# Optimization experiments

Hardware: AMD Instinct MI355X
Metric: run time of the kernel (lower is better)

## Reference

```python
import jax, jax.numpy as jnp
import numpy as np

DIM = 192
HEADS = 8
EPS = 1e-12

def conv2d(x, w, groups=1, padding='SAME'):
    return jax.lax.conv_general_dilated(
        x, w, window_strides=(1, 1), padding=padding,
        dimension_numbers=('NCHW', 'OIHW', 'NCHW'),
        feature_group_count=groups)

def setup_inputs() -> dict:
    key = jax.random.key(0)
    ks = jax.random.split(key, 6)
    b, c, h, w = 8, DIM, 128, 128
    x = jax.random.normal(ks[0], (b, c, h, w), dtype=jnp.float32)
    # depthwise 3x3 conv on x (groups=dim): OIHW with I=1
    w_dw = jax.random.normal(ks[1], (DIM, 1, 3, 3), dtype=jnp.float32) * 0.1
    # 1x1 qkv projection
    w_qkv = jax.random.normal(ks[2], (DIM * 3, DIM, 1, 1), dtype=jnp.float32) * (1.0 / np.sqrt(DIM))
    # depthwise 3x3 on qkv (groups=3*dim)
    w_qkvdw = jax.random.normal(ks[3], (DIM * 3, 1, 3, 3), dtype=jnp.float32) * 0.1
    # 1x1 output projection
    w_proj = jax.random.normal(ks[4], (DIM, DIM, 1, 1), dtype=jnp.float32) * (1.0 / np.sqrt(DIM))
    temperature = jnp.ones((HEADS, 1, 1), dtype=jnp.float32)
    rescale = jnp.ones((HEADS, 1), dtype=jnp.float32)
    return {"x": x, "w_dw": w_dw, "w_qkv": w_qkv, "w_qkvdw": w_qkvdw,
            "w_proj": w_proj, "temperature": temperature, "rescale": rescale}

def l2norm_lastdim(t):
    # matches F.normalize(t, dim=-1, eps=1e-12)
    n = jnp.sqrt(jnp.sum(t * t, axis=-1, keepdims=True))
    return t / jnp.maximum(n, EPS)

def reference(x, w_dw, w_qkv, w_qkvdw, w_proj, temperature, rescale):
    b, c, h, w = x.shape
    heads = HEADS
    c_head = c // heads
    # variance (unbiased, like torch.var default) of depthwise-conv features over H,W
    xd = conv2d(x, w_dw, groups=c)                      # [b,c,h,w]
    var = jnp.var(xd, axis=(-2, -1), ddof=1)            # [b,c]
    var = var.reshape(b, heads, c_head)                 # [b,head,c_head]
    # qkv: 1x1 conv then depthwise 3x3
    qkv = conv2d(conv2d(x, w_qkv), w_qkvdw, groups=3 * c)  # [b,3c,h,w]
    q, k, v = jnp.split(qkv, 3, axis=1)
    def to_heads(t):
        return t.reshape(b, heads, c_head, h * w)       # b head c (h w)
    q, k, v = to_heads(q), to_heads(k), to_heads(v)
    q = l2norm_lastdim(q)
    k = l2norm_lastdim(k)
    # channel attention: [b,head,c_head,c_head]
    attn = jnp.einsum('bhcn,bhdn->bhcd', q, k) * temperature
    # diagonal bias from variance, scaled per-head
    diag = rescale * var                                # [b,head,c_head]
    attn = attn + jnp.einsum('bhc,cd->bhcd', diag, jnp.eye(c_head, dtype=attn.dtype))
    attn = jax.nn.softmax(attn, axis=-1)
    out = jnp.einsum('bhcd,bhdn->bhcn', attn, v)        # [b,head,c_head,hw]
    out = out.reshape(b, c, h, w)
    return conv2d(out, w_proj)
```

## Files before the change

kernel.cpp:

```cpp
#include <hip/hip_runtime.h>
#include <hip/hip_bf16.h>

typedef unsigned short ushort_t;
typedef __bf16 bf16x8 __attribute__((ext_vector_type(8)));
typedef float f32x4 __attribute__((ext_vector_type(4)));
typedef unsigned short us8 __attribute__((ext_vector_type(8)));
typedef unsigned short us4 __attribute__((ext_vector_type(4)));

#define HW 16384
#define CDIM 192
#define QKVC 576

static __device__ __forceinline__ float b2f(unsigned short u) {
    union { unsigned int i; float f; } cv; cv.i = ((unsigned int)u) << 16; return cv.f;
}
static __device__ __forceinline__ unsigned short f2b(float f) {
    union { __bf16 h; unsigned short u; } cv; cv.h = (__bf16)f; return cv.u;
}

__global__ __launch_bounds__(256) void k_cvt(const float* __restrict__ src,
                                             ushort_t* __restrict__ dst, int n8) {
    int i = blockIdx.x * 256 + threadIdx.x;
    if (i >= n8) return;
    f32x4 a = *(const f32x4*)&src[i * 8];
    f32x4 b = *(const f32x4*)&src[i * 8 + 4];
    us8 o;
#pragma unroll
    for (int e = 0; e < 4; ++e) { o[e] = f2b(a[e]); o[4 + e] = f2b(b[e]); }
    *(us8*)&dst[i * 8] = o;
}

__global__ __launch_bounds__(256) void k_dwvar(const float* __restrict__ x,
                                               const float* __restrict__ wdw,
                                               float* __restrict__ vs1,
                                               float* __restrict__ vs2,
                                               ushort_t* __restrict__ xb) {
    __shared__ __align__(16) float pl[66 * 132];
    __shared__ float red[8];
    int blk = blockIdx.x;
    int bc = blk >> 1, half = blk & 1, rb = half * 64;
    int c = bc % CDIM;
    const float* xp = x + (size_t)bc * HW;
    ushort_t* xbp = xb + (size_t)bc * HW;
    int t = threadIdx.x;
#pragma unroll
    for (int i = 0; i < 8; ++i) {
        int gi = t + i * 256;
        int row = gi >> 5, q4 = (gi & 31) * 4;
        f32x4 v4 = *(const f32x4*)&xp[(size_t)(rb + row) * 128 + q4];
        *(f32x4*)&pl[(row + 1) * 132 + q4] = v4;
        us4 b4;
#pragma unroll
        for (int j = 0; j < 4; ++j) b4[j] = f2b(v4[j]);
        *(us4*)&xbp[(size_t)(rb + row) * 128 + q4] = b4;
    }
    if (t < 32) {
        f32x4 v = {0.f, 0.f, 0.f, 0.f};
        if (rb > 0) v = *(const f32x4*)&xp[(size_t)(rb - 1) * 128 + t * 4];
        *(f32x4*)&pl[t * 4] = v;
    } else if (t < 64) {
        int g = t - 32;
        f32x4 v = {0.f, 0.f, 0.f, 0.f};
        if (rb + 64 < 128) v = *(const f32x4*)&xp[(size_t)(rb + 64) * 128 + g * 4];
        *(f32x4*)&pl[65 * 132 + g * 4] = v;
    }
    float w[9];
#pragma unroll
    for (int j = 0; j < 9; ++j) w[j] = wdw[c * 9 + j];
    __syncthreads();

    int lane = t & 63, wv = t >> 6;
    int y = lane, xs = wv * 32;
    int yb0 = y * 132, yb1 = yb0 + 132, yb2 = yb1 + 132;
    float l0 = 0.f, l1 = 0.f, l2 = 0.f;
    if (xs != 0) {
        f32x4 h0 = *(const f32x4*)&pl[yb0 + xs - 4];
        f32x4 h1 = *(const f32x4*)&pl[yb1 + xs - 4];
        f32x4 h2 = *(const f32x4*)&pl[yb2 + xs - 4];
        l0 = h0[3]; l1 = h1[3]; l2 = h2[3];
    }
    f32x4 a0 = *(const f32x4*)&pl[yb0 + xs], b0 = *(const f32x4*)&pl[yb0 + xs + 4];
    f32x4 a1 = *(const f32x4*)&pl[yb1 + xs], b1 = *(const f32x4*)&pl[yb1 + xs + 4];
    f32x4 a2 = *(const f32x4*)&pl[yb2 + xs], b2 = *(const f32x4*)&pl[yb2 + xs + 4];
    float s1 = 0.f, s2 = 0.f;
#pragma unroll
    for (int g = 0; g < 4; ++g) {
        int x0 = xs + g * 8;
        f32x4 na0, nb0, na1, nb1, na2, nb2;
        float e9_0, e9_1, e9_2;
        if (g < 3) {
            na0 = *(const f32x4*)&pl[yb0 + x0 + 8]; nb0 = *(const f32x4*)&pl[yb0 + x0 + 12];
            na1 = *(const f32x4*)&pl[yb1 + x0 + 8]; nb1 = *(const f32x4*)&pl[yb1 + x0 + 12];
            na2 = *(const f32x4*)&pl[yb2 + x0 + 8]; nb2 = *(const f32x4*)&pl[yb2 + x0 + 12];
            e9_0 = na0[0]; e9_1 = na1[0]; e9_2 = na2[0];
        } else {
            e9_0 = e9_1 = e9_2 = 0.f;
            if (xs + 32 < 128) {
                f32x4 q0 = *(const f32x4*)&pl[yb0 + xs + 32];
                f32x4 q1 = *(const f32x4*)&pl[yb1 + xs + 32];
                f32x4 q2 = *(const f32x4*)&pl[yb2 + xs + 32];
                e9_0 = q0[0]; e9_1 = q1[0]; e9_2 = q2[0];
            }
        }
        float e0[10], e1[10], e2[10];
        e0[0] = l0; e1[0] = l1; e2[0] = l2;
#pragma unroll
        for (int j = 0; j < 4; ++j) {
            e0[1 + j] = a0[j]; e0[5 + j] = b0[j];
            e1[1 + j] = a1[j]; e1[5 + j] = b1[j];
            e2[1 + j] = a2[j]; e2[5 + j] = b2[j];
        }
        e0[9] = e9_0; e1[9] = e9_1; e2[9] = e9_2;
#pragma unroll
        for (int j = 0; j < 8; ++j) {
            float o = e0[j] * w[0] + e0[j + 1] * w[1] + e0[j + 2] * w[2]
                    + e1[j] * w[3] + e1[j + 1] * w[4] + e1[j + 2] * w[5]
                    + e2[j] * w[6] + e2[j + 1] * w[7] + e2[j + 2] * w[8];
            s1 += o; s2 += o * o;
        }
        l0 = e0[8]; l1 = e1[8]; l2 = e2[8];
        if (g < 3) { a0 = na0; b0 = nb0; a1 = na1; b1 = nb1; a2 = na2; b2 = nb2; }
    }
#pragma unroll
    for (int off = 32; off; off >>= 1) { s1 += __shfl_xor(s1, off); s2 += __shfl_xor(s2, off); }
    if (lane == 0) { red[wv * 2] = s1; red[wv * 2 + 1] = s2; }
    __syncthreads();
    if (t == 0) {
        atomicAdd(&vs1[bc], red[0] + red[2] + red[4] + red[6]);
        atomicAdd(&vs2[bc], red[1] + red[3] + red[5] + red[7]);
    }
}

__global__ __launch_bounds__(256) void k_dwqkv(const ushort_t* __restrict__ qkvraw,
                                               const float* __restrict__ wqd,
                                               ushort_t* __restrict__ qkvd,
                                               float* __restrict__ ssq) {
    __shared__ __align__(16) ushort_t pl[66 * 136];
    __shared__ float red[4];
    int blk = blockIdx.x;
    int bo = blk >> 1, half = blk & 1, rb = half * 64;
    int o = bo % QKVC, b = bo / QKVC;
    const ushort_t* xp = qkvraw + (size_t)bo * HW;
    ushort_t* op = qkvd + (size_t)bo * HW;
    int t = threadIdx.x;
#pragma unroll
    for (int i = 0; i < 4; ++i) {
        int gi = t + i * 256;
        int row = gi >> 4, gr = (gi & 15) * 8;
        *(us8*)&pl[(row + 1) * 136 + gr] = *(const us8*)&xp[(size_t)(rb + row) * 128 + gr];
    }
    if (t < 16) {
        us8 v = {};
        if (rb > 0) v = *(const us8*)&xp[(size_t)(rb - 1) * 128 + t * 8];
        *(us8*)&pl[t * 8] = v;
    } else if (t < 32) {
        int g = t - 16;
        us8 v = {};
        if (rb + 64 < 128) v = *(const us8*)&xp[(size_t)(rb + 64) * 128 + g * 8];
        *(us8*)&pl[65 * 136 + g * 8] = v;
    }
    float w[9];
#pragma unroll
    for (int j = 0; j < 9; ++j) w[j] = wqd[o * 9 + j];
    __syncthreads();

    int lane = t & 63, wv = t >> 6;
    int y = lane, xs = wv * 32;
    int yb0 = y * 136, yb1 = yb0 + 136, yb2 = yb1 + 136;
    float l0 = 0.f, l1 = 0.f, l2 = 0.f;
    if (xs != 0) {
        us8 h0 = *(const us8*)&pl[yb0 + xs - 8];
        us8 h1 = *(const us8*)&pl[yb1 + xs - 8];
        us8 h2 = *(const us8*)&pl[yb2 + xs - 8];
        l0 = b2f(h0[7]); l1 = b2f(h1[7]); l2 = b2f(h2[7]);
    }
    us8 c0 = *(const us8*)&pl[yb0 + xs];
    us8 c1 = *(const us8*)&pl[yb1 + xs];
    us8 c2 = *(const us8*)&pl[yb2 + xs];
    float s2 = 0.f;
#pragma unroll
    for (int g = 0; g < 4; ++g) {
        int x0 = xs + g * 8;
        us8 n0, n1, n2;
        float e9_0, e9_1, e9_2;
        if (g < 3) {
            n0 = *(const us8*)&pl[yb0 + x0 + 8];
            n1 = *(const us8*)&pl[yb1 + x0 + 8];
            n2 = *(const us8*)&pl[yb2 + x0 + 8];
            e9_0 = b2f(n0[0]); e9_1 = b2f(n1[0]); e9_2 = b2f(n2[0]);
        } else {
            e9_0 = e9_1 = e9_2 = 0.f;
            if (xs + 32 < 128) {
                us8 q0 = *(const us8*)&pl[yb0 + xs + 32];
                us8 q1 = *(const us8*)&pl[yb1 + xs + 32];
                us8 q2 = *(const us8*)&pl[yb2 + xs + 32];
                e9_0 = b2f(q0[0]); e9_1 = b2f(q1[0]); e9_2 = b2f(q2[0]);
            }
        }
        float e0[10], e1[10], e2[10];
        e0[0] = l0; e1[0] = l1; e2[0] = l2;
#pragma unroll
        for (int j = 0; j < 8; ++j) { e0[j + 1] = b2f(c0[j]); e1[j + 1] = b2f(c1[j]); e2[j + 1] = b2f(c2[j]); }
        e0[9] = e9_0; e1[9] = e9_1; e2[9] = e9_2;
        us8 ob;
#pragma unroll
        for (int j = 0; j < 8; ++j) {
            float ov = e0[j] * w[0] + e0[j + 1] * w[1] + e0[j + 2] * w[2]
                     + e1[j] * w[3] + e1[j + 1] * w[4] + e1[j + 2] * w[5]
                     + e2[j] * w[6] + e2[j + 1] * w[7] + e2[j + 2] * w[8];
            ob[j] = f2b(ov);
            s2 += ov * ov;
        }
        *(us8*)&op[(size_t)(rb + y) * 128 + x0] = ob;
        l0 = e0[8]; l1 = e1[8]; l2 = e2[8];
        if (g < 3) { c0 = n0; c1 = n1; c2 = n2; }
    }
#pragma unroll
    for (int off = 32; off; off >>= 1) s2 += __shfl_xor(s2, off);
    if (lane == 0) red[wv] = s2;
    __syncthreads();
    if (t == 0 && o < 2 * CDIM)
        atomicAdd(&ssq[b * 384 + o], red[0] + red[1] + red[2] + red[3]);
}

template<int CF>
__global__ __launch_bounds__(256) void k_gemm(const ushort_t* __restrict__ Av, long sAb,
                                              const ushort_t* __restrict__ Bv, long sBb,
                                              void* __restrict__ Cv, long sCb, int K) {
    __shared__ __align__(16) char smem[49152];
    ushort_t* As = (ushort_t*)smem;
    ushort_t* Bs = (ushort_t*)(smem + 24576);
    int t = threadIdx.x;
    int wv = t >> 6, lane = t & 63, quad = lane >> 4, l15 = lane & 15;
    size_t aoff = (size_t)blockIdx.z * sAb + (size_t)blockIdx.y * 192 * K;
    size_t boff = (size_t)blockIdx.z * sBb + (size_t)blockIdx.x * 128;
    size_t coff = (size_t)blockIdx.z * sCb + (size_t)blockIdx.y * 192 * HW + (size_t)blockIdx.x * 128;
    f32x4 acc[24] = {};
    int bkr = t >> 3, bn0 = (t & 7) * 16, tlow = t & 7;
    int gk0 = bkr >> 3, klo = bkr & 7;
    const ushort_t* Bp = Bv + boff;
    us8 pb0 = *(const us8*)&Bp[(size_t)bkr * HW + bn0];
    us8 pb1 = *(const us8*)&Bp[(size_t)bkr * HW + bn0 + 8];
    us8 pb2 = *(const us8*)&Bp[(size_t)(bkr + 32) * HW + bn0];
    us8 pb3 = *(const us8*)&Bp[(size_t)(bkr + 32) * HW + bn0 + 8];
    int nIter = K >> 6;
    for (int it = 0; it < nIter; ++it) {
        int kk = it << 6;
#pragma unroll
        for (int i = 0; i < 6; ++i) {
            int s = t + i * 256;
            int row = s >> 3, kc = (s & 7) * 8;
            int kcs = kc ^ ((row & 7) * 8);
            *(uint4*)&As[row * 64 + kcs] = *(const uint4*)&Av[aoff + (size_t)row * K + kk + kc];
        }
#pragma unroll
        for (int e = 0; e < 8; ++e) {
            int col0 = ((gk0 ^ tlow ^ e) << 3) + klo;
            Bs[(bn0 + e) * 64 + col0] = pb0[e];
            Bs[(bn0 + 8 + e) * 64 + col0] = pb1[e];
            int col1 = (((gk0 + 4) ^ tlow ^ e) << 3) + klo;
            Bs[(bn0 + e) * 64 + col1] = pb2[e];
            Bs[(bn0 + 8 + e) * 64 + col1] = pb3[e];
        }
        __syncthreads();
        if (it + 1 < nIter) {
            const ushort_t* Bn = &Bp[(size_t)(kk + 64) * HW];
            pb0 = *(const us8*)&Bn[(size_t)bkr * HW + bn0];
            pb1 = *(const us8*)&Bn[(size_t)bkr * HW + bn0 + 8];
            pb2 = *(const us8*)&Bn[(size_t)(bkr + 32) * HW + bn0];
            pb3 = *(const us8*)&Bn[(size_t)(bkr + 32) * HW + bn0 + 8];
        }
#pragma unroll
        for (int s = 0; s < 2; ++s) {
            int r0 = wv * 16 + l15, r1 = 64 + r0, r2 = 128 + r0;
            int ko = s * 32 + quad * 8;
            bf16x8 af0 = *(const bf16x8*)&As[r0 * 64 + (ko ^ ((r0 & 7) * 8))];
            bf16x8 af1 = *(const bf16x8*)&As[r1 * 64 + (ko ^ ((r1 & 7) * 8))];
            bf16x8 af2 = *(const bf16x8*)&As[r2 * 64 + (ko ^ ((r2 & 7) * 8))];
#pragma unroll
            for (int tc = 0; tc < 8; ++tc) {
                int n = tc * 16 + l15;
                int g = (s * 4 + quad) ^ ((tc ^ l15) & 7);
                bf16x8 bfr = *(const bf16x8*)&Bs[n * 64 + (g << 3)];
                acc[tc]      = __builtin_amdgcn_mfma_f32_16x16x32_bf16(af0, bfr, acc[tc],      0, 0, 0);
                acc[8 + tc]  = __builtin_amdgcn_mfma_f32_16x16x32_bf16(af1, bfr, acc[8 + tc],  0, 0, 0);
                acc[16 + tc] = __builtin_amdgcn_mfma_f32_16x16x32_bf16(af2, bfr, acc[16 + tc], 0, 0, 0);
            }
        }
        __syncthreads();
    }
    if (CF == 0) {
        ushort_t* Ct = (ushort_t*)smem;
#pragma unroll
        for (int rt = 0; rt < 3; ++rt)
#pragma unroll
            for (int tc = 0; tc < 8; ++tc)
#pragma unroll
                for (int r = 0; r < 4; ++r)
                    Ct[(rt * 64 + wv * 16 + quad * 4 + r) * 128 + tc * 16 + l15] = f2b(acc[rt * 8 + tc][r]);
        __syncthreads();
        ushort_t* Co = (ushort_t*)Cv;
#pragma unroll
        for (int i = 0; i < 12; ++i) {
            int s = t + i * 256;
            int row = s >> 4, c8 = (s & 15) * 8;
            *(us8*)&Co[coff + (size_t)row * HW + c8] = *(us8*)&Ct[row * 128 + c8];
        }
    } else {
        float* Cf = (float*)smem;
        float* Co = (float*)Cv;
#pragma unroll
        for (int rt = 0; rt < 3; ++rt) {
            if (rt) __syncthreads();
#pragma unroll
            for (int tc = 0; tc < 8; ++tc)
#pragma unroll
                for (int r = 0; r < 4; ++r)
                    Cf[(wv * 16 + quad * 4 + r) * 128 + tc * 16 + l15] = acc[rt * 8 + tc][r];
            __syncthreads();
#pragma unroll
            for (int i = 0; i < 8; ++i) {
                int s = t + i * 256;
                int row = s >> 5, c4 = (s & 31) * 4;
                *(f32x4*)&Co[coff + (size_t)(rt * 64 + row) * HW + c4] = *(f32x4*)&Cf[row * 128 + c4];
            }
        }
    }
}

__global__ __launch_bounds__(256) void k_gram(const ushort_t* __restrict__ qkvd,
                                              float* __restrict__ G) {
    __shared__ __align__(16) ushort_t qs[24 * 264];
    __shared__ __align__(16) ushort_t ks[24 * 264];
    int bh = blockIdx.y;
    int b = bh >> 3, h = bh & 7;
    int t = threadIdx.x, wv = t >> 6, lane = t & 63, quad = lane >> 4, l15 = lane & 15;
    const ushort_t* qb = qkvd + (size_t)b * 9437184 + (size_t)(h * 24) * HW;
    const ushort_t* kp = qb + (size_t)CDIM * HW;
    f32x4 a00 = {}, a01 = {}, a10 = {}, a11 = {};
    bf16x8 z = {};
    bool hi = (l15 < 8);
    int kbase0 = blockIdx.x * 2048;
    for (int sub = 0; sub < 8; ++sub) {
        int kbase = kbase0 + sub * 256;
#pragma unroll
        for (int j = 0; j < 3; ++j) {
            int gi = t + j * 256;
            int row = gi >> 5, c8 = (gi & 31) * 8;
            *(us8*)&qs[row * 264 + c8] = *(const us8*)&qb[(size_t)row * HW + kbase + c8];
            *(us8*)&ks[row * 264 + c8] = *(const us8*)&kp[(size_t)row * HW + kbase + c8];
        }
        __syncthreads();
#pragma unroll
        for (int s = 0; s < 2; ++s) {
            int ko = (wv * 2 + s) * 32 + quad * 8;
            bf16x8 qa0 = *(const bf16x8*)&qs[l15 * 264 + ko];
            bf16x8 qa1 = hi ? *(const bf16x8*)&qs[(16 + l15) * 264 + ko] : z;
            bf16x8 kb0 = *(const bf16x8*)&ks[l15 * 264 + ko];
            bf16x8 kb1 = hi ? *(const bf16x8*)&ks[(16 + l15) * 264 + ko] : z;
            a00 = __builtin_amdgcn_mfma_f32_16x16x32_bf16(qa0, kb0, a00, 0, 0, 0);
            a01 = __builtin_amdgcn_mfma_f32_16x16x32_bf16(qa0, kb1, a01, 0, 0, 0);
            a10 = __builtin_amdgcn_mfma_f32_16x16x32_bf16(qa1, kb0, a10, 0, 0, 0);
            a11 = __builtin_amdgcn_mfma_f32_16x16x32_bf16(qa1, kb1, a11, 0, 0, 0);
        }
        __syncthreads();
    }
    float* Gp = G + (size_t)bh * 576;
#pragma unroll
    for (int r = 0; r < 4; ++r) {
        int r0 = quad * 4 + r, r1 = 16 + quad * 4 + r;
        int c0 = l15, c1 = 16 + l15;
        atomicAdd(&Gp[r0 * 24 + c0], a00[r]);
        if (c1 < 24) atomicAdd(&Gp[r0 * 24 + c1], a01[r]);
        if (r1 < 24) atomicAdd(&Gp[r1 * 24 + c0], a10[r]);
        if (r1 < 24 && c1 < 24) atomicAdd(&Gp[r1 * 24 + c1], a11[r]);
    }
}

__global__ __launch_bounds__(256) void k_smweff(const float* __restrict__ G,
                                                const float* __restrict__ ssq,
                                                const float* __restrict__ vs1,
                                                const float* __restrict__ vs2,
                                                const float* __restrict__ wproj,
                                                const float* __restrict__ temp,
                                                const float* __restrict__ resc,
                                                ushort_t* __restrict__ Weff) {
    int b = blockIdx.x, t = threadIdx.x;
    __shared__ float P[8 * 24 * 24];
    __shared__ float snq[192], snk[192];
    if (t < 192) {
        snq[t] = fmaxf(sqrtf(ssq[b * 384 + t]), 1e-12f);
        snk[t] = fmaxf(sqrtf(ssq[b * 384 + 192 + t]), 1e-12f);
    }
    __syncthreads();
    if (t < 192) {
        int h = t / 24, c = t % 24;
        float tmpv = temp[h];
        float S1 = vs1[b * 192 + t], S2 = vs2[b * 192 + t];
        float varv = (S2 - S1 * S1 * (1.0f / 16384.f)) * (1.0f / 16383.f);
        float dvar = resc[h] * varv;
        const float* Gp = G + (size_t)(b * 8 + h) * 576 + c * 24;
        float inq = tmpv / snq[t];
        float lg[24]; float mx = -1e30f;
#pragma unroll
        for (int d = 0; d < 24; ++d) {
            float v = Gp[d] * inq / snk[h * 24 + d];
            if (d == c) v += dvar;
            lg[d] = v; mx = fmaxf(mx, v);
        }
        float sum = 0.f;
#pragma unroll
        for (int d = 0; d < 24; ++d) { float e = __expf(lg[d] - mx); lg[d] = e; sum += e; }
        float inv = 1.f / sum;
#pragma unroll
        for (int d = 0; d < 24; ++d) P[(h * 24 + c) * 24 + d] = lg[d] * inv;
    }
    __syncthreads();
#pragma unroll
    for (int i = 0; i < 6; ++i) {
        int idx = t + (blockIdx.y * 6 + i) * 256;
        int co = idx / 192, hd = idx % 192;
        int h2 = hd / 24, d = hd % 24;
        float a = 0.f;
#pragma unroll
        for (int c2 = 0; c2 < 24; ++c2)
            a += wproj[co * 192 + h2 * 24 + c2] * P[(h2 * 24 + c2) * 24 + d];
        Weff[(size_t)b * 36864 + idx] = f2b(a);
    }
}

extern "C" void kernel_launch(void* const* d_in, const int* in_sizes, int n_in,
                              void* d_out, int out_size, void* d_ws, size_t ws_size,
                              hipStream_t stream) {
    const float* x      = (const float*)d_in[0];
    const float* wdw    = (const float*)d_in[1];
    const float* wqkv   = (const float*)d_in[2];
    const float* wqkvdw = (const float*)d_in[3];
    const float* wproj  = (const float*)d_in[4];
    const float* temp   = (const float*)d_in[5];
    const float* resc   = (const float*)d_in[6];
    float* out = (float*)d_out;

    char* ws = (char*)d_ws;
    ushort_t* qkvraw = (ushort_t*)ws;
    ushort_t* qkvd   = (ushort_t*)(ws + 150994944);
    char* small = ws + 301989888;
    float* vs1  = (float*)small;
    float* vs2  = (float*)(small + 6144);
    float* ssq  = (float*)(small + 12288);
    float* G    = (float*)(small + 24576);
    ushort_t* Weff = (ushort_t*)(small + 172032);

    ushort_t* xb  = qkvd;
    ushort_t* wqb = qkvd + 60000000;

    (void)hipMemsetAsync(small, 0, 172032, stream);
    k_cvt<<<dim3(54), dim3(256), 0, stream>>>(wqkv, wqb, 13824);
    k_dwvar<<<dim3(3072), dim3(256), 0, stream>>>(x, wdw, vs1, vs2, xb);
    k_gemm<0><<<dim3(128, 3, 8), dim3(256), 0, stream>>>(wqb, 0L, xb, 3145728L, qkvraw, 9437184L, 192);
    k_dwqkv<<<dim3(9216), dim3(256), 0, stream>>>(qkvraw, wqkvdw, qkvd, ssq);
    k_gram<<<dim3(8, 64), dim3(256), 0, stream>>>(qkvd, G);
    k_smweff<<<dim3(8, 24), dim3(256), 0, stream>>>(G, ssq, vs1, vs2, wproj, temp, resc, Weff);
    k_gemm<1><<<dim3(128, 1, 8), dim3(256), 0, stream>>>(Weff, 36864L, qkvd + (size_t)384 * HW, 9437184L, out, 3145728L, 192);
}
```

Before: 362.7 us.

## Fuse q/k depthwise conv into Gram kernel, restrict dwconv pass to v

The depthwise 3x3 conv for q and k channels now runs inside the Gram-matrix kernel, which loads row bands with halo from the raw qkv buffer, convolves them in shared memory, accumulates sum-of-squares, and feeds MFMA directly. The separate depthwise kernel now only processes the v third of the channels. This removes the write and re-read of the convolved q/k tensors (about two thirds of the dwconv output traffic) in exchange for halo reloads, shared-memory atomics and more syncs per band in the fused kernel.

Result: slower. 391.5 us (+7.9%).

```diff
diff --git a/kernel.cpp b/kernel.cpp
--- a/kernel.cpp
+++ b/kernel.cpp
@@ -131,15 +131,15 @@
     }
 }
 
-__global__ __launch_bounds__(256) void k_dwqkv(const ushort_t* __restrict__ qkvraw,
-                                               const float* __restrict__ wqd,
-                                               ushort_t* __restrict__ qkvd,
-                                               float* __restrict__ ssq) {
+__global__ __launch_bounds__(256) void k_dwv(const ushort_t* __restrict__ qkvraw,
+                                             const float* __restrict__ wqd,
+                                             ushort_t* __restrict__ qkvd) {
     __shared__ __align__(16) ushort_t pl[66 * 136];
-    __shared__ float red[4];
     int blk = blockIdx.x;
-    int bo = blk >> 1, half = blk & 1, rb = half * 64;
-    int o = bo % QKVC, b = bo / QKVC;
+    int pv = blk >> 1, half = blk & 1, rb = half * 64;
+    int b = pv / 192, ol = pv - b * 192;
+    int o = 384 + ol;
+    int bo = b * 576 + o;
     const ushort_t* xp = qkvraw + (size_t)bo * HW;
     ushort_t* op = qkvd + (size_t)bo * HW;
     int t = threadIdx.x;
@@ -177,7 +177,6 @@
     us8 c0 = *(const us8*)&pl[yb0 + xs];
     us8 c1 = *(const us8*)&pl[yb1 + xs];
     us8 c2 = *(const us8*)&pl[yb2 + xs];
-    float s2 = 0.f;
 #pragma unroll
     for (int g = 0; g < 4; ++g) {
         int x0 = xs + g * 8;
@@ -209,18 +208,127 @@
                      + e1[j] * w[3] + e1[j + 1] * w[4] + e1[j + 2] * w[5]
                      + e2[j] * w[6] + e2[j + 1] * w[7] + e2[j + 2] * w[8];
             ob[j] = f2b(ov);
-            s2 += ov * ov;
         }
         *(us8*)&op[(size_t)(rb + y) * 128 + x0] = ob;
         l0 = e0[8]; l1 = e1[8]; l2 = e2[8];
         if (g < 3) { c0 = n0; c1 = n1; c2 = n2; }
     }
-#pragma unroll
-    for (int off = 32; off; off >>= 1) s2 += __shfl_xor(s2, off);
-    if (lane == 0) red[wv] = s2;
+}
+
+__global__ __launch_bounds__(256) void k_qkgram(const ushort_t* __restrict__ qkvraw,
+                                                const float* __restrict__ wqd,
+                                                float* __restrict__ G,
+                                                float* __restrict__ ssq) {
+    __shared__ __align__(16) ushort_t in[48 * 4 * 128];
+    __shared__ float wl[48 * 9];
+    __shared__ float ssql[48];
+    ushort_t* qt = in;
+    ushort_t* kt = in + 24 * 264;
+    int band = blockIdx.x;
+    int bh = blockIdx.y;
+    int b = bh >> 3, h = bh & 7;
+    int t = threadIdx.x, wv = t >> 6, lane = t & 63, quad = lane >> 4, l15 = lane & 15;
+    bool hi = (l15 < 8);
+    bf16x8 z = {};
+    f32x4 a00 = {}, a01 = {}, a10 = {}, a11 = {};
+    if (t < 48) ssql[t] = 0.f;
+    for (int j = t; j < 432; j += 256) {
+        int p = j / 9, kk = j - p * 9;
+        int o = (p < 24) ? (h * 24 + p) : (192 + h * 24 + (p - 24));
+        wl[j] = wqd[o * 9 + kk];
+    }
+    const ushort_t* base = qkvraw + (size_t)b * 9437184;
+
+    for (int it2 = 0; it2 < 4; ++it2) {
+        __syncthreads();
+        int r0 = band * 8 + it2 * 2;
+#pragma unroll
+        for (int i = 0; i < 12; ++i) {
+            int gg = t + i * 256;
+            int p = gg >> 6, rem = gg & 63, ri = rem >> 4, gx = rem & 15;
+            int o = (p < 24) ? (h * 24 + p) : (192 + h * 24 + (p - 24));
+            int gr = r0 - 1 + ri;
+            us8 v = {};
+            if (gr >= 0 && gr < 128)
+                v = *(const us8*)&base[(size_t)o * HW + (size_t)gr * 128 + gx * 8];
+            *(us8*)&in[(p * 4 + ri) * 128 + gx * 8] = v;
+        }
+        __syncthreads();
+        us8 pa0, pa1, pa2, pa3, pa4, pa5;
+#pragma unroll
+        for (int i = 0; i < 6; ++i) {
+            int g = t + i * 256;
+            int s = g >> 4, p = s >> 1, orow = s & 1, x0 = (g & 15) * 8;
+            int rb0 = (p * 4 + orow) * 128;
+            us8 v0 = *(const us8*)&in[rb0 + x0];
+            us8 v1 = *(const us8*)&in[rb0 + 128 + x0];
+            us8 v2 = *(const us8*)&in[rb0 + 256 + x0];
+            float e0[10], e1[10], e2[10];
+            e0[0] = (x0 > 0) ? b2f(in[rb0 + x0 - 1]) : 0.f;
+            e1[0] = (x0 > 0) ? b2f(in[rb0 + 128 + x0 - 1]) : 0.f;
+            e2[0] = (x0 > 0) ? b2f(in[rb0 + 256 + x0 - 1]) : 0.f;
+#pragma unroll
+            for (int j = 0; j < 8; ++j) { e0[j + 1] = b2f(v0[j]); e1[j + 1] = b2f(v1[j]); e2[j + 1] = b2f(v2[j]); }
+            e0[9] = (x0 < 120) ? b2f(in[rb0 + x0 + 8]) : 0.f;
+            e1[9] = (x0 < 120) ? b2f(in[rb0 + 128 + x0 + 8]) : 0.f;
+            e2[9] = (x0 < 120) ? b2f(in[rb0 + 256 + x0 + 8]) : 0.f;
+            float w0 = wl[p * 9 + 0], w1 = wl[p * 9 + 1], w2 = wl[p * 9 + 2];
+            float w3 = wl[p * 9 + 3], w4 = wl[p * 9 + 4], w5 = wl[p * 9 + 5];
+            float w6 = wl[p * 9 + 6], w7 = wl[p * 9 + 7], w8 = wl[p * 9 + 8];
+            us8 ob;
+            float s2g = 0.f;
+#pragma unroll
+            for (int j = 0; j < 8; ++j) {
+                float ov = e0[j] * w0 + e0[j + 1] * w1 + e0[j + 2] * w2
+                         + e1[j] * w3 + e1[j + 1] * w4 + e1[j + 2] * w5
+                         + e2[j] * w6 + e2[j + 1] * w7 + e2[j + 2] * w8;
+                ob[j] = f2b(ov);
+                s2g += ov * ov;
+            }
+            atomicAdd(&ssql[p], s2g);
+            if (i == 0) pa0 = ob; else if (i == 1) pa1 = ob; else if (i == 2) pa2 = ob;
+            else if (i == 3) pa3 = ob; else if (i == 4) pa4 = ob; else pa5 = ob;
+        }
+        __syncthreads();
+#pragma unroll
+        for (int i = 0; i < 6; ++i) {
+            int g = t + i * 256;
+            int s = g >> 4, p = s >> 1, orow = s & 1, x0 = (g & 15) * 8;
+            us8 ob = (i == 0) ? pa0 : (i == 1) ? pa1 : (i == 2) ? pa2
+                   : (i == 3) ? pa3 : (i == 4) ? pa4 : pa5;
+            ushort_t* dst = (p < 24) ? qt : kt;
+            int cc = (p < 24) ? p : (p - 24);
+            *(us8*)&dst[cc * 264 + orow * 128 + x0] = ob;
+        }
+        __syncthreads();
+#pragma unroll
+        for (int s = 0; s < 2; ++s) {
+            int ko = (wv * 2 + s) * 32 + quad * 8;
+            bf16x8 qa0 = *(const bf16x8*)&qt[l15 * 264 + ko];
+            bf16x8 qa1 = hi ? *(const bf16x8*)&qt[(16 + l15) * 264 + ko] : z;
+            bf16x8 kb0 = *(const bf16x8*)&kt[l15 * 264 + ko];
+            bf16x8 kb1 = hi ? *(const bf16x8*)&kt[(16 + l15) * 264 + ko] : z;
+            a00 = __builtin_amdgcn_mfma_f32_16x16x32_bf16(qa0, kb0, a00, 0, 0, 0);
+            a01 = __builtin_amdgcn_mfma_f32_16x16x32_bf16(qa0, kb1, a01, 0, 0, 0);
+            a10 = __builtin_amdgcn_mfma_f32_16x16x32_bf16(qa1, kb0, a10, 0, 0, 0);
+            a11 = __builtin_amdgcn_mfma_f32_16x16x32_bf16(qa1, kb1, a11, 0, 0, 0);
+        }
+    }
+    float* Gp = G + (size_t)bh * 576;
+#pragma unroll
+    for (int r = 0; r < 4; ++r) {
+        int rr0 = quad * 4 + r, rr1 = 16 + quad * 4 + r;
+        int cc0 = l15, cc1 = 16 + l15;
+        atomicAdd(&Gp[rr0 * 24 + cc0], a00[r]);
+        if (cc1 < 24) atomicAdd(&Gp[rr0 * 24 + cc1], a01[r]);
+        if (rr1 < 24) atomicAdd(&Gp[rr1 * 24 + cc0], a10[r]);
+        if (rr1 < 24 && cc1 < 24) atomicAdd(&Gp[rr1 * 24 + cc1], a11[r]);
+    }
     __syncthreads();
-    if (t == 0 && o < 2 * CDIM)
-        atomicAdd(&ssq[b * 384 + o], red[0] + red[1] + red[2] + red[3]);
+    if (t < 48) {
+        int idx = (t < 24) ? (b * 384 + h * 24 + t) : (b * 384 + 192 + h * 24 + (t - 24));
+        atomicAdd(&ssq[idx], ssql[t]);
+    }
 }
 
 template<int CF>
@@ -328,55 +436,6 @@
     }
 }
 
-__global__ __launch_bounds__(256) void k_gram(const ushort_t* __restrict__ qkvd,
-                                              float* __restrict__ G) {
-    __shared__ __align__(16) ushort_t qs[24 * 264];
-    __shared__ __align__(16) ushort_t ks[24 * 264];
-    int bh = blockIdx.y;
-    int b = bh >> 3, h = bh & 7;
-    int t = threadIdx.x, wv = t >> 6, lane = t & 63, quad = lane >> 4, l15 = lane & 15;
-    const ushort_t* qb = qkvd + (size_t)b * 9437184 + (size_t)(h * 24) * HW;
-    const ushort_t* kp = qb + (size_t)CDIM * HW;
-    f32x4 a00 = {}, a01 = {}, a10 = {}, a11 = {};
-    bf16x8 z = {};
-    bool hi = (l15 < 8);
-    int kbase0 = blockIdx.x * 2048;
-    for (int sub = 0; sub < 8; ++sub) {
-        int kbase = kbase0 + sub * 256;
-#pragma unroll
-        for (int j = 0; j < 3; ++j) {
-            int gi = t + j * 256;
-            int row = gi >> 5, c8 = (gi & 31) * 8;
-            *(us8*)&qs[row * 264 + c8] = *(const us8*)&qb[(size_t)row * HW + kbase + c8];
-            *(us8*)&ks[row * 264 + c8] = *(const us8*)&kp[(size_t)row * HW + kbase + c8];
-        }
-        __syncthreads();
-#pragma unroll
-        for (int s = 0; s < 2; ++s) {
-            int ko = (wv * 2 + s) * 32 + quad * 8;
-            bf16x8 qa0 = *(const bf16x8*)&qs[l15 * 264 + ko];
-            bf16x8 qa1 = hi ? *(const bf16x8*)&qs[(16 + l15) * 264 + ko] : z;
-            bf16x8 kb0 = *(const bf16x8*)&ks[l15 * 264 + ko];
-            bf16x8 kb1 = hi ? *(const bf16x8*)&ks[(16 + l15) * 264 + ko] : z;
-            a00 = __builtin_amdgcn_mfma_f32_16x16x32_bf16(qa0, kb0, a00, 0, 0, 0);
-            a01 = __builtin_amdgcn_mfma_f32_16x16x32_bf16(qa0, kb1, a01, 0, 0, 0);
-            a10 = __builtin_amdgcn_mfma_f32_16x16x32_bf16(qa1, kb0, a10, 0, 0, 0);
-            a11 = __builtin_amdgcn_mfma_f32_16x16x32_bf16(qa1, kb1, a11, 0, 0, 0);
-        }
-        __syncthreads();
-    }
-    float* Gp = G + (size_t)bh * 576;
-#pragma unroll
-    for (int r = 0; r < 4; ++r) {
-        int r0 = quad * 4 + r, r1 = 16 + quad * 4 + r;
-        int c0 = l15, c1 = 16 + l15;
-        atomicAdd(&Gp[r0 * 24 + c0], a00[r]);
-        if (c1 < 24) atomicAdd(&Gp[r0 * 24 + c1], a01[r]);
-        if (r1 < 24) atomicAdd(&Gp[r1 * 24 + c0], a10[r]);
-        if (r1 < 24 && c1 < 24) atomicAdd(&Gp[r1 * 24 + c1], a11[r]);
-    }
-}
-
 __global__ __launch_bounds__(256) void k_smweff(const float* __restrict__ G,
                                                 const float* __restrict__ ssq,
                                                 const float* __restrict__ vs1,
@@ -458,8 +517,8 @@
     k_cvt<<<dim3(54), dim3(256), 0, stream>>>(wqkv, wqb, 13824);
     k_dwvar<<<dim3(3072), dim3(256), 0, stream>>>(x, wdw, vs1, vs2, xb);
     k_gemm<0><<<dim3(128, 3, 8), dim3(256), 0, stream>>>(wqb, 0L, xb, 3145728L, qkvraw, 9437184L, 192);
-    k_dwqkv<<<dim3(9216), dim3(256), 0, stream>>>(qkvraw, wqkvdw, qkvd, ssq);
-    k_gram<<<dim3(8, 64), dim3(256), 0, stream>>>(qkvd, G);
+    k_dwv<<<dim3(3072), dim3(256), 0, stream>>>(qkvraw, wqkvdw, qkvd);
+    k_qkgram<<<dim3(16, 64), dim3(256), 0, stream>>>(qkvraw, wqkvdw, G, ssq);
     k_smweff<<<dim3(8, 24), dim3(256), 0, stream>>>(G, ssq, vs1, vs2, wproj, temp, resc, Weff);
     k_gemm<1><<<dim3(128, 1, 8), dim3(256), 0, stream>>>(Weff, 36864L, qkvd + (size_t)384 * HW, 9437184L, out, 3145728L, 192);
 }
```
